# Optimization experiments

Measured on AMD Instinct MI355X. Metric: run time of the kernel, lower is better.

Reference implementation:

```python
import jax, jax.numpy as jnp
import numpy as np

INV_SQRT_2PI = 1.0 / np.sqrt(2.0 * np.pi)
EPS = 1e-15


def setup_inputs() -> dict:
    key = jax.random.key(0)
    k1, k2, k3 = jax.random.split(key, 3)
    n = 8192
    # m_z: network outputs [g1, g2]
    m_z = 0.5 * jax.random.normal(k1, (n, 2), dtype=jnp.float32)
    # y: strictly positive survival times (rand, shifted away from 0 for log)
    y = jax.random.uniform(k2, (n, 1), dtype=jnp.float32, minval=0.05, maxval=5.0)
    delta = (jax.random.uniform(k3, (n, 1), dtype=jnp.float32) < 0.7).astype(jnp.float32)
    return {"m_z": m_z, "y": y, "delta": delta}


def reference(m_z, y, delta):
    n = m_z.shape[0]
    g1 = m_z[:, 0:1]                      # [n,1]
    g2 = m_z[:, 1:2]                      # [n,1]
    h = 1.3 * float(n) ** (-0.2)          # bandwidth
    R = g1 + jnp.log(y)                   # [n,1]
    d = delta[:, 0]                       # [n]

    S1 = jnp.sum(delta * g2) / n
    S2 = -jnp.sum(delta * R) / n

    DR = (R - R.T) / h                    # [n,n] pairwise (R_i - R_j)/h
    # Gaussian kernel pdf, column-reduced with delta weights
    K = jnp.exp(-0.5 * DR * DR) * INV_SQRT_2PI
    Dk = (d @ K) / (n * h)                # [n] : sum_i delta_i K_ij / (n h)
    S3 = jnp.sum(d * jnp.log(Dk + EPS)) / n

    # Gaussian cdf, column-reduced with L = exp(g2-g1) weights
    P = jax.scipy.special.ndtr(DR)        # [n,n]
    L = jnp.exp(g2 - g1)[:, 0]            # [n]
    LP_sum = (L @ P) / n                  # [n]
    S4 = -jnp.sum(d * jnp.log(LP_sum + EPS)) / n

    return -(S1 + S2 + S3 + S4)
```

## Files before the change

kernel.cpp:

```cpp
#include <hip/hip_runtime.h>
#include <math.h>

#define TPB 256
#define IB 64
#define EPSF 1e-15f

__global__ __launch_bounds__(TPB, 8) void pair_kernel(
    const float* __restrict__ m_z, const float* __restrict__ y,
    const float* __restrict__ delta, float2* __restrict__ P,
    float* __restrict__ out, float inv_hk, int n, int span) {
    __shared__ float4 sRd[128];
    __shared__ float2 sL2[128];
    __shared__ float sLtot;
    const int tid = threadIdx.x;
    const int j = blockIdx.x * TPB + tid;
    const float2* __restrict__ mz2 = (const float2*)m_z;

    const float2 gj = mz2[j];
    const float Rj = (gj.x + __logf(y[j])) * inv_hk;

    const int ibase = blockIdx.y * span;
    if (tid < span) {
        const int i = ibase + tid;
        const float2 g = mz2[i];
        float* s = (float*)sRd;
        const int pk = tid >> 1, hf = tid & 1;
        s[4 * pk + hf]     = (g.x + __logf(y[i])) * inv_hk;
        s[4 * pk + 2 + hf] = delta[i];
        ((float*)sL2)[tid] = __expf(g.y - g.x);
    }
    __syncthreads();
    if (tid < 64) {
        float s = 0.0f;
        for (int t = tid; t < span; t += 64) s += ((float*)sL2)[t];
        for (int o = 32; o > 0; o >>= 1) s += __shfl_down(s, o, 64);
        if (tid == 0) sLtot = s;
    }
    __syncthreads();
    if (j == 0 && blockIdx.y == 0) out[0] = 0.0f;

    float a0 = 0.0f, a1 = 0.0f, b0 = 0.5f * sLtot, b1 = 0.0f;
    const int m = span >> 1;
#pragma unroll 4
    for (int k = 0; k < m; ++k) {
        const float4 rd = sRd[k];
        const float2 ll = sL2[k];
        const float dr0 = rd.x - Rj;
        const float dr1 = rd.y - Rj;
        const float e0 = __builtin_amdgcn_exp2f(-(dr0 * dr0));
        const float e1 = __builtin_amdgcn_exp2f(-(dr1 * dr1));
        const float t0 = __builtin_amdgcn_rcpf(fmaf(0.3916993f, fabsf(dr0), 1.0f));
        const float t1 = __builtin_amdgcn_rcpf(fmaf(0.3916993f, fabsf(dr1), 1.0f));
        const float u0 = t0 * fmaf(t0, fmaf(t0, 0.3739278f, -0.0479399f), 0.1740121f) * e0;
        const float u1 = t1 * fmaf(t1, fmaf(t1, 0.3739278f, -0.0479399f), 0.1740121f) * e1;
        a0 = fmaf(rd.z, e0, a0);
        a1 = fmaf(rd.w, e1, a1);
        b0 = fmaf(copysignf(ll.x, dr0), 0.5f - u0, b0);
        b1 = fmaf(copysignf(ll.y, dr1), 0.5f - u1, b1);
    }
    P[(size_t)blockIdx.y * n + j] = make_float2(a0 + a1, b0 + b1);
}

__global__ __launch_bounds__(TPB) void finalize_kernel(
    const float2* __restrict__ P, const float* __restrict__ m_z,
    const float* __restrict__ y, const float* __restrict__ delta,
    float* __restrict__ out, float c1, float invn, int n) {
    const int j = blockIdx.x * TPB + threadIdx.x;
    float sa = 0.0f, sb = 0.0f;
    for (int b = 0; b < IB; ++b) {
        const float2 v = P[(size_t)b * n + j];
        sa += v.x;
        sb += v.y;
    }
    const float d = delta[j];
    const float R = m_z[2 * j] + __logf(y[j]);
    float term = d * (R - m_z[2 * j + 1] - __logf(fmaf(c1, sa, EPSF))
                                         + __logf(fmaf(invn, sb, EPSF)));
    for (int o = 32; o > 0; o >>= 1) term += __shfl_down(term, o, 64);
    __shared__ float wsum[TPB / 64];
    if ((threadIdx.x & 63) == 0) wsum[threadIdx.x >> 6] = term;
    __syncthreads();
    if (threadIdx.x == 0) {
        float ssum = 0.0f;
        for (int w = 0; w < TPB / 64; ++w) ssum += wsum[w];
        atomicAdd(out, ssum * invn);
    }
}

extern "C" void kernel_launch(void* const* d_in, const int* in_sizes, int n_in,
                              void* d_out, int out_size, void* d_ws, size_t ws_size,
                              hipStream_t stream) {
    const float* m_z   = (const float*)d_in[0];
    const float* y     = (const float*)d_in[1];
    const float* delta = (const float*)d_in[2];
    float* out = (float*)d_out;
    const int n = in_sizes[1];

    float2* P = (float2*)d_ws;

    const double h = 1.3 * pow((double)n, -0.2);
    const double k = 1.1774100225154747;
    const float inv_hk = (float)(1.0 / (h * k));
    const float c1 = (float)(0.3989422804014327 / ((double)n * h));
    const float invn = 1.0f / (float)n;
    const int span = n / IB;

    const int nblk = (n + TPB - 1) / TPB;
    dim3 grid(nblk, IB);
    pair_kernel<<<grid, TPB, 0, stream>>>(m_z, y, delta, P, out, inv_hk, n, span);
    finalize_kernel<<<nblk, TPB, 0, stream>>>(P, m_z, y, delta, out, c1, invn, n);
}
```

Before: 82.64 us.

## Broadcast i-tile via readlane registers instead of LDS staging

Each wavefront now loads its own 128-element i-slice into registers and broadcasts each element with readlane (scalar registers), removing LDS stores, both __syncthreads barriers and per-iteration LDS reads. Delta is packed into the sign of L, so each element needs only two broadcasts. The cost is that every wave redundantly recomputes log/exp for the slice, plus extra compare/select and fabs work in the inner loop. The two-way accumulator ILP is reduced to a single chain, and the loop is hard-coded to 128 elements (2x64), which quietly assumes span==128.

```diff
diff --git a/kernel.cpp b/kernel.cpp
--- a/kernel.cpp
+++ b/kernel.cpp
@@ -9,56 +9,53 @@
     const float* __restrict__ m_z, const float* __restrict__ y,
     const float* __restrict__ delta, float2* __restrict__ P,
     float* __restrict__ out, float inv_hk, int n, int span) {
-    __shared__ float4 sRd[128];
-    __shared__ float2 sL2[128];
-    __shared__ float sLtot;
     const int tid = threadIdx.x;
+    const int lane = tid & 63;
     const int j = blockIdx.x * TPB + tid;
     const float2* __restrict__ mz2 = (const float2*)m_z;
+
+    if (j == 0 && blockIdx.y == 0) out[0] = 0.0f;
 
     const float2 gj = mz2[j];
     const float Rj = (gj.x + __logf(y[j])) * inv_hk;
 
     const int ibase = blockIdx.y * span;
-    if (tid < span) {
-        const int i = ibase + tid;
+    float vR[2], vV[2];
+    float lsum = 0.0f;
+#pragma unroll
+    for (int r = 0; r < 2; ++r) {
+        const int i = ibase + r * 64 + lane;
         const float2 g = mz2[i];
-        float* s = (float*)sRd;
-        const int pk = tid >> 1, hf = tid & 1;
-        s[4 * pk + hf]     = (g.x + __logf(y[i])) * inv_hk;
-        s[4 * pk + 2 + hf] = delta[i];
-        ((float*)sL2)[tid] = __expf(g.y - g.x);
+        vR[r] = (g.x + __logf(y[i])) * inv_hk;
+        const float L = __expf(g.y - g.x);
+        vV[r] = (delta[i] != 0.0f) ? -L : L;
+        lsum += L;
     }
-    __syncthreads();
-    if (tid < 64) {
-        float s = 0.0f;
-        for (int t = tid; t < span; t += 64) s += ((float*)sL2)[t];
-        for (int o = 32; o > 0; o >>= 1) s += __shfl_down(s, o, 64);
-        if (tid == 0) sLtot = s;
+    for (int o = 32; o > 0; o >>= 1) lsum += __shfl_xor(lsum, o, 64);
+
+    float accA = 0.0f;
+    float accB = 0.5f * lsum;
+#pragma unroll
+    for (int r = 0; r < 2; ++r) {
+#pragma unroll 16
+        for (int k = 0; k < 64; ++k) {
+            const float sR = __int_as_float(
+                __builtin_amdgcn_readlane(__float_as_int(vR[r]), k));
+            const float sV = __int_as_float(
+                __builtin_amdgcn_readlane(__float_as_int(vV[r]), k));
+            const float sd = (sV < 0.0f) ? 1.0f : 0.0f;
+            const float sL = fabsf(sV);
+            const float dr = sR - Rj;
+            const float q = dr * dr;
+            const float e = __builtin_amdgcn_exp2f(-q);
+            const float t = __builtin_amdgcn_rcpf(fmaf(0.3916993f, fabsf(dr), 1.0f));
+            const float u = t * fmaf(t, fmaf(t, 0.3739278f, -0.0479399f),
+                                     0.1740121f) * e;
+            accA = fmaf(sd, e, accA);
+            accB = fmaf(copysignf(sL, dr), 0.5f - u, accB);
+        }
     }
-    __syncthreads();
-    if (j == 0 && blockIdx.y == 0) out[0] = 0.0f;
-
-    float a0 = 0.0f, a1 = 0.0f, b0 = 0.5f * sLtot, b1 = 0.0f;
-    const int m = span >> 1;
-#pragma unroll 4
-    for (int k = 0; k < m; ++k) {
-        const float4 rd = sRd[k];
-        const float2 ll = sL2[k];
-        const float dr0 = rd.x - Rj;
-        const float dr1 = rd.y - Rj;
-        const float e0 = __builtin_amdgcn_exp2f(-(dr0 * dr0));
-        const float e1 = __builtin_amdgcn_exp2f(-(dr1 * dr1));
-        const float t0 = __builtin_amdgcn_rcpf(fmaf(0.3916993f, fabsf(dr0), 1.0f));
-        const float t1 = __builtin_amdgcn_rcpf(fmaf(0.3916993f, fabsf(dr1), 1.0f));
-        const float u0 = t0 * fmaf(t0, fmaf(t0, 0.3739278f, -0.0479399f), 0.1740121f) * e0;
-        const float u1 = t1 * fmaf(t1, fmaf(t1, 0.3739278f, -0.0479399f), 0.1740121f) * e1;
-        a0 = fmaf(rd.z, e0, a0);
-        a1 = fmaf(rd.w, e1, a1);
-        b0 = fmaf(copysignf(ll.x, dr0), 0.5f - u0, b0);
-        b1 = fmaf(copysignf(ll.y, dr1), 0.5f - u1, b1);
-    }
-    P[(size_t)blockIdx.y * n + j] = make_float2(a0 + a1, b0 + b1);
+    P[(size_t)blockIdx.y * n + j] = make_float2(accA, accB);
 }
 
 __global__ __launch_bounds__(TPB) void finalize_kernel(
@@ -99,8 +96,8 @@
     float2* P = (float2*)d_ws;
 
     const double h = 1.3 * pow((double)n, -0.2);
-    const double k = 1.1774100225154747;
-    const float inv_hk = (float)(1.0 / (h * k));
+    const double kk = 1.1774100225154747;
+    const float inv_hk = (float)(1.0 / (h * kk));
     const float c1 = (float)(0.3989422804014327 / ((double)n * h));
     const float invn = 1.0f / (float)n;
     const int span = n / IB;
```

After: 99.11 us. 1.2x slower.

## Replace hardware rcp with Newton bit-trick reciprocal, 4-way unroll with compile-time span

Applied to the files above, without the earlier changes.

The inner pair loop now computes 1/(1+p|x|) from a magic-constant initial guess refined by two Newton steps, in place of the hardware rcp instruction. It also processes four pairs per iteration with four independent accumulator pairs, reads R, delta and L from separate float4 LDS arrays, and specializes the kernel on a compile-time span of 128. The aim is to move work off the transcendental unit onto plain FMA instructions and expose more instruction-level parallelism. The cost is more VALU instructions per pair and higher register pressure.

```diff
diff --git a/kernel.cpp b/kernel.cpp
--- a/kernel.cpp
+++ b/kernel.cpp
@@ -5,16 +5,19 @@
 #define IB 64
 #define EPSF 1e-15f
 
+template <int SPAN>
 __global__ __launch_bounds__(TPB, 8) void pair_kernel(
     const float* __restrict__ m_z, const float* __restrict__ y,
     const float* __restrict__ delta, float2* __restrict__ P,
-    float* __restrict__ out, float inv_hk, int n, int span) {
-    __shared__ float4 sRd[128];
-    __shared__ float2 sL2[128];
+    float* __restrict__ out, float inv_hk, int n, int span_rt) {
+    const int span = SPAN ? SPAN : span_rt;
+    __shared__ float sR[256], sD[256], sL[256];
     __shared__ float sLtot;
     const int tid = threadIdx.x;
     const int j = blockIdx.x * TPB + tid;
     const float2* __restrict__ mz2 = (const float2*)m_z;
+
+    if (j == 0 && blockIdx.y == 0) out[0] = 0.0f;
 
     const float2 gj = mz2[j];
     const float Rj = (gj.x + __logf(y[j])) * inv_hk;
@@ -23,42 +26,53 @@
     if (tid < span) {
         const int i = ibase + tid;
         const float2 g = mz2[i];
-        float* s = (float*)sRd;
-        const int pk = tid >> 1, hf = tid & 1;
-        s[4 * pk + hf]     = (g.x + __logf(y[i])) * inv_hk;
-        s[4 * pk + 2 + hf] = delta[i];
-        ((float*)sL2)[tid] = __expf(g.y - g.x);
+        sR[tid] = (g.x + __logf(y[i])) * inv_hk;
+        sD[tid] = delta[i];
+        sL[tid] = __expf(g.y - g.x);
     }
     __syncthreads();
     if (tid < 64) {
         float s = 0.0f;
-        for (int t = tid; t < span; t += 64) s += ((float*)sL2)[t];
+        for (int t = tid; t < span; t += 64) s += sL[t];
         for (int o = 32; o > 0; o >>= 1) s += __shfl_down(s, o, 64);
         if (tid == 0) sLtot = s;
     }
     __syncthreads();
-    if (j == 0 && blockIdx.y == 0) out[0] = 0.0f;
 
-    float a0 = 0.0f, a1 = 0.0f, b0 = 0.5f * sLtot, b1 = 0.0f;
-    const int m = span >> 1;
-#pragma unroll 4
+    const float4* __restrict__ sR4 = (const float4*)sR;
+    const float4* __restrict__ sD4 = (const float4*)sD;
+    const float4* __restrict__ sL4 = (const float4*)sL;
+
+    float a0 = 0, a1 = 0, a2 = 0, a3 = 0;
+    float b0 = 0.5f * sLtot, b1 = 0, b2 = 0, b3 = 0;
+    const int m = span >> 2;
+#pragma unroll 8
     for (int k = 0; k < m; ++k) {
-        const float4 rd = sRd[k];
-        const float2 ll = sL2[k];
-        const float dr0 = rd.x - Rj;
-        const float dr1 = rd.y - Rj;
-        const float e0 = __builtin_amdgcn_exp2f(-(dr0 * dr0));
-        const float e1 = __builtin_amdgcn_exp2f(-(dr1 * dr1));
-        const float t0 = __builtin_amdgcn_rcpf(fmaf(0.3916993f, fabsf(dr0), 1.0f));
-        const float t1 = __builtin_amdgcn_rcpf(fmaf(0.3916993f, fabsf(dr1), 1.0f));
-        const float u0 = t0 * fmaf(t0, fmaf(t0, 0.3739278f, -0.0479399f), 0.1740121f) * e0;
-        const float u1 = t1 * fmaf(t1, fmaf(t1, 0.3739278f, -0.0479399f), 0.1740121f) * e1;
-        a0 = fmaf(rd.z, e0, a0);
-        a1 = fmaf(rd.w, e1, a1);
-        b0 = fmaf(copysignf(ll.x, dr0), 0.5f - u0, b0);
-        b1 = fmaf(copysignf(ll.y, dr1), 0.5f - u1, b1);
+        const float4 R4 = sR4[k];
+        const float4 D4 = sD4[k];
+        const float4 L4 = sL4[k];
+#define PAIR(p, ACC_A, ACC_B)                                                  \
+    {                                                                          \
+        const float dr = R4.p - Rj;                                            \
+        const float q = dr * dr;                                               \
+        const float e = __builtin_amdgcn_exp2f(-q);     \
+        const float a = fmaf(0.3916993f, fabsf(dr), 1.0f);                     \
+        float t = __int_as_float(0x7EF127EAu - __float_as_int(a));             \
+        t = t * fmaf(-a, t, 2.0f);                               \
+        t = t * fmaf(-a, t, 2.0f);                \
+        const float u = t * fmaf(t, fmaf(t, 0.3739278f, -0.0479399f),          \
+                                 0.1740121f) * e;                              \
+        ACC_A = fmaf(D4.p, e, ACC_A);                                          \
+        ACC_B = fmaf(copysignf(L4.p, dr), 0.5f - u, ACC_B);                    \
     }
-    P[(size_t)blockIdx.y * n + j] = make_float2(a0 + a1, b0 + b1);
+        PAIR(x, a0, b0)
+        PAIR(y, a1, b1)
+        PAIR(z, a2, b2)
+        PAIR(w, a3, b3)
+#undef PAIR
+    }
+    P[(size_t)blockIdx.y * n + j] =
+        make_float2((a0 + a1) + (a2 + a3), (b0 + b1) + (b2 + b3));
 }
 
 __global__ __launch_bounds__(TPB) void finalize_kernel(
@@ -99,14 +113,19 @@
     float2* P = (float2*)d_ws;
 
     const double h = 1.3 * pow((double)n, -0.2);
-    const double k = 1.1774100225154747;
-    const float inv_hk = (float)(1.0 / (h * k));
+    const double kk = 1.1774100225154747;
+    const float inv_hk = (float)(1.0 / (h * kk));
     const float c1 = (float)(0.3989422804014327 / ((double)n * h));
     const float invn = 1.0f / (float)n;
     const int span = n / IB;
 
     const int nblk = (n + TPB - 1) / TPB;
     dim3 grid(nblk, IB);
-    pair_kernel<<<grid, TPB, 0, stream>>>(m_z, y, delta, P, out, inv_hk, n, span);
+    if (span == 128)
+        pair_kernel<128><<<grid, TPB, 0, stream>>>(m_z, y, delta, P, out,
+                                                   inv_hk, n, span);
+    else
+        pair_kernel<0><<<grid, TPB, 0, stream>>>(m_z, y, delta, P, out,
+                                                 inv_hk, n, span);
     finalize_kernel<<<nblk, TPB, 0, stream>>>(P, m_z, y, delta, out, c1, invn, n);
 }
```

After: 90.37 us. 9.4% more time.
